# Kernel optimization log

Measured on AMD Instinct MI355X. Metric: run time of the kernel, lower is better.

Reference implementation:

```python
import jax, jax.numpy as jnp
import numpy as np

T = 4096      # total tokens (flattened batch)
H = 4096      # input_size / hidden dim
O = 4096      # output_size_per_partition
R = 16        # max_lora_rank
L = 8         # max_loras
S = 8         # num_lora_seqs


def setup_inputs() -> dict:
    key = jax.random.key(0)
    k_x, k_w, k_b, k_a, k_bb, k_idx = jax.random.split(key, 6)
    x = jax.random.normal(k_x, (T, H), dtype=jnp.float32)
    weight = jax.random.normal(k_w, (O, H), dtype=jnp.float32) * 0.02
    bias = jax.random.normal(k_b, (O,), dtype=jnp.float32)
    lora_a = jax.random.normal(k_a, (L, H, R), dtype=jnp.float32) * 0.02
    lora_b = jax.random.normal(k_bb, (L, R, O), dtype=jnp.float32) * 0.02
    # indices[i] = (start_idx[i], lora_idx[i]); indices[-1,0] = T (end sentinel).
    # Segment i covers tokens [start[i], start[i+1]) and uses adapter lora_idx[i].
    starts = jnp.arange(S + 1, dtype=jnp.int64) * (T // S)  # monotonically increasing, covers [0, T]
    lora_ids = jax.random.randint(k_idx, (S + 1,), 0, L).astype(jnp.int64)
    indices = jnp.stack([starts, lora_ids], axis=1)  # [S+1, 2]
    return {"x": x, "weight": weight, "bias": bias,
            "lora_a": lora_a, "lora_b": lora_b, "indices": indices}


def reference(x, weight, bias, lora_a, lora_b, indices):
    # Base ColumnParallelLinear: y = x @ W^T + b
    out = jnp.dot(x, weight.T) + bias  # [T, O]

    # Map each token to the LoRA adapter of its segment (SGMV semantics).
    starts = indices[:-1, 0]      # [S]
    seg_lora = indices[:-1, 1]    # [S]
    tok = jnp.arange(x.shape[0])
    seg_of_tok = jnp.searchsorted(starts, tok, side="right") - 1  # [T]
    tok_lora = seg_lora[seg_of_tok]                               # [T]

    # Grouped low-rank GEMM: out[t] += x[t] @ A[lora(t)] @ B[lora(t)].
    # Loop over the small fixed adapter set; mask selects each adapter's tokens.
    n_loras = lora_a.shape[0]
    for l in range(n_loras):
        mask = (tok_lora == l).astype(x.dtype)[:, None]  # [T, 1]
        u = jnp.dot(x * mask, lora_a[l])                 # [T, R] (zero rows off-adapter)
        out = out + jnp.dot(u, lora_b[l])                # [T, O]
    return out
```

## Files before the change

kernel.cpp:

```cpp
#include <hip/hip_runtime.h>
#include <hip/hip_bf16.h>
#include <stdint.h>

#define T_DIM 4096
#define H_DIM 4096
#define O_DIM 4096
#define R_DIM 16
#define S_SEG 8

typedef __attribute__((ext_vector_type(8))) short bf16x8_t;
typedef __attribute__((ext_vector_type(4))) float f32x4_t;

struct ushort4_t { unsigned short x, y, z, w; };

__device__ __forceinline__ unsigned short f2bf(float f) {
  union { float f; unsigned int u; } v; v.f = f;
  unsigned int u = v.u;
  unsigned int r = (u + 0x7fffu + ((u >> 16) & 1u)) >> 16;
  return (unsigned short)r;
}

__device__ __forceinline__ void gload16(const void* g, void* l) {
  __builtin_amdgcn_global_load_lds(
      (const __attribute__((address_space(1))) unsigned int*)g,
      (__attribute__((address_space(3))) unsigned int*)l,
      16, 0, 0);
}

__device__ __forceinline__ int lora_of(const int* __restrict__ indices, int t) {
  int seg = 0;
#pragma unroll
  for (int s = 1; s < S_SEG; ++s)
    if (indices[2 * s] <= t) seg = s;
  return indices[2 * seg + 1];
}

#define SBAR() do { asm volatile("" ::: "memory"); __builtin_amdgcn_s_barrier(); asm volatile("" ::: "memory"); } while (0)
#define VMCNT8() asm volatile("s_waitcnt vmcnt(8)" ::: "memory")
#define VMCNT0() asm volatile("s_waitcnt vmcnt(0)" ::: "memory")

__global__ __launch_bounds__(256) void cvt_kernel(const float* __restrict__ in,
                                                  unsigned short* __restrict__ out,
                                                  int n) {
  int i = (blockIdx.x * 256 + threadIdx.x) * 8;
  if (i >= n) return;
  float4 a = *(const float4*)(in + i);
  float4 b = *(const float4*)(in + i + 4);
  union { unsigned short s[8]; bf16x8_t v; } r;
  r.s[0] = f2bf(a.x); r.s[1] = f2bf(a.y); r.s[2] = f2bf(a.z); r.s[3] = f2bf(a.w);
  r.s[4] = f2bf(b.x); r.s[5] = f2bf(b.y); r.s[6] = f2bf(b.z); r.s[7] = f2bf(b.w);
  *(bf16x8_t*)(out + i) = r.v;
}

__global__ __launch_bounds__(256) void transpose_a(const float* __restrict__ a,
                                                   float* __restrict__ aT) {
  int l = blockIdx.y;
  const float* al = a + (size_t)l * H_DIM * R_DIM;
  float* aTl = aT + (size_t)l * H_DIM * R_DIM;
  int base = blockIdx.x * 4096;
  for (int idx = base + threadIdx.x; idx < base + 4096; idx += 256) {
    int h = idx >> 4, r = idx & 15;
    aTl[r * H_DIM + h] = al[idx];
  }
}

__global__ __launch_bounds__(256) void fused_x_kernel(const float* __restrict__ x,
                                                      const float* __restrict__ aT,
                                                      const int* __restrict__ indices,
                                                      unsigned short* __restrict__ Xb,
                                                      float* __restrict__ u) {
  const int t0 = blockIdx.x * 4;
  const int tid = threadIdx.x;
  const int l = lora_of(indices, t0);
  const float* __restrict__ aTl = aT + (size_t)l * H_DIM * R_DIM;

  float acc[4][16];
#pragma unroll
  for (int t = 0; t < 4; ++t)
#pragma unroll
    for (int r = 0; r < 16; ++r) acc[t][r] = 0.f;

#pragma unroll
  for (int c = 0; c < 4; ++c) {
    const int h = c * 1024 + tid * 4;
    union { float4 v; float f[4]; } xv[4];
#pragma unroll
    for (int t = 0; t < 4; ++t)
      xv[t].v = *(const float4*)(x + (size_t)(t0 + t) * H_DIM + h);
#pragma unroll
    for (int t = 0; t < 4; ++t) {
      ushort4_t o;
      o.x = f2bf(xv[t].f[0]); o.y = f2bf(xv[t].f[1]);
      o.z = f2bf(xv[t].f[2]); o.w = f2bf(xv[t].f[3]);
      *(ushort4_t*)(Xb + (size_t)(t0 + t) * H_DIM + h) = o;
    }
#pragma unroll
    for (int r = 0; r < 16; ++r) {
      float4 av = *(const float4*)(aTl + (size_t)r * H_DIM + h);
#pragma unroll
      for (int t = 0; t < 4; ++t)
        acc[t][r] += xv[t].f[0] * av.x + xv[t].f[1] * av.y +
                     xv[t].f[2] * av.z + xv[t].f[3] * av.w;
    }
  }

#pragma unroll
  for (int t = 0; t < 4; ++t)
#pragma unroll
    for (int r = 0; r < 16; ++r)
#pragma unroll
      for (int off = 32; off > 0; off >>= 1)
        acc[t][r] += __shfl_xor(acc[t][r], off, 64);

  __shared__ float red[4][64];
  const int lane = tid & 63, wv = tid >> 6;
  if (lane == 0) {
#pragma unroll
    for (int t = 0; t < 4; ++t)
#pragma unroll
      for (int r = 0; r < 16; ++r) red[wv][t * 16 + r] = acc[t][r];
  }
  __syncthreads();
  if (tid < 64) {
    float s = red[0][tid] + red[1][tid] + red[2][tid] + red[3][tid];
    u[(size_t)t0 * 16 + tid] = s;
  }
}

__global__ __launch_bounds__(512) void gemm256(const unsigned short* __restrict__ A,
                                               const unsigned short* __restrict__ B,
                                               const float* __restrict__ bias,
                                               const float* __restrict__ lora_b,
                                               const int* __restrict__ indices,
                                               const float* __restrict__ u,
                                               float* __restrict__ out) {
  extern __shared__ unsigned short lds[];
  const int tid = threadIdx.x;
  const int lane = tid & 63;
  const int wid = tid >> 6;
  const int wr = wid >> 2;
  const int wc = wid & 3;
  const int row0 = blockIdx.y * 256;
  const int col0 = blockIdx.x * 256;

  f32x4_t acc[8][4];
#pragma unroll
  for (int m = 0; m < 8; ++m)
#pragma unroll
    for (int n = 0; n < 4; ++n) acc[m][n] = (f32x4_t){0.f, 0.f, 0.f, 0.f};

  const int srow = tid >> 3;
  const int kbyte = ((tid & 7) * 16) ^ (((tid >> 5) & 1) << 5);
  const unsigned short* aS0 = A + (size_t)(row0 + 0 * 64 + srow) * H_DIM + (kbyte >> 1);
  const unsigned short* aS1 = A + (size_t)(row0 + 1 * 64 + srow) * H_DIM + (kbyte >> 1);
  const unsigned short* aS2 = A + (size_t)(row0 + 2 * 64 + srow) * H_DIM + (kbyte >> 1);
  const unsigned short* aS3 = A + (size_t)(row0 + 3 * 64 + srow) * H_DIM + (kbyte >> 1);
  const unsigned short* bS0 = B + (size_t)(col0 + 0 * 64 + srow) * H_DIM + (kbyte >> 1);
  const unsigned short* bS1 = B + (size_t)(col0 + 1 * 64 + srow) * H_DIM + (kbyte >> 1);
  const unsigned short* bS2 = B + (size_t)(col0 + 2 * 64 + srow) * H_DIM + (kbyte >> 1);
  const unsigned short* bS3 = B + (size_t)(col0 + 3 * 64 + srow) * H_DIM + (kbyte >> 1);

#define STAGE(kt, d) do {                                                  \
    unsigned short* La_ = lds + (d) * 16384;                               \
    unsigned short* Lb_ = lds + 32768 + (d) * 16384;                       \
    gload16(aS0 + (kt), La_ + tid * 8);                                    \
    gload16(aS1 + (kt), La_ + 4096 + tid * 8);                             \
    gload16(aS2 + (kt), La_ + 8192 + tid * 8);                             \
    gload16(aS3 + (kt), La_ + 12288 + tid * 8);                            \
    gload16(bS0 + (kt), Lb_ + tid * 8);                                    \
    gload16(bS1 + (kt), Lb_ + 4096 + tid * 8);                             \
    gload16(bS2 + (kt), Lb_ + 8192 + tid * 8);                             \
    gload16(bS3 + (kt), Lb_ + 12288 + tid * 8);                            \
  } while (0)

  const int rA = wr * 128 + (lane & 15);
  const int rB = wc * 64 + (lane & 15);
  const int aBase = rA * 64;
  const int bBase = rB * 64;
  const int ks0 = ((((lane >> 4) * 16)) ^ ((lane & 4) << 3)) >> 1;
  const int ks1 = (((64 + (lane >> 4) * 16)) ^ ((lane & 4) << 3)) >> 1;

  STAGE(0, 0);
  STAGE(64, 1);
  VMCNT8();
  SBAR();

#pragma unroll 2
  for (int t = 0; t < H_DIM / 64; ++t) {
    const int cur = t & 1;
    const unsigned short* La = lds + cur * 16384;
    const unsigned short* Lb = lds + 32768 + cur * 16384;

    bf16x8_t b0, b1, b2, b3, a0, a1, a2, a3;
    b0 = *(const bf16x8_t*)(Lb + bBase + 0 * 1024 + ks0);
    b1 = *(const bf16x8_t*)(Lb + bBase + 1 * 1024 + ks0);
    b2 = *(const bf16x8_t*)(Lb + bBase + 2 * 1024 + ks0);
    b3 = *(const bf16x8_t*)(Lb + bBase + 3 * 1024 + ks0);
    a0 = *(const bf16x8_t*)(La + aBase + 0 * 1024 + ks0);
    a1 = *(const bf16x8_t*)(La + aBase + 1 * 1024 + ks0);
    a2 = *(const bf16x8_t*)(La + aBase + 2 * 1024 + ks0);
    a3 = *(const bf16x8_t*)(La + aBase + 3 * 1024 + ks0);
    __builtin_amdgcn_s_setprio(1);
    acc[0][0] = __builtin_amdgcn_mfma_f32_16x16x32_bf16(a0, b0, acc[0][0], 0, 0, 0);
    acc[0][1] = __builtin_amdgcn_mfma_f32_16x16x32_bf16(a0, b1, acc[0][1], 0, 0, 0);
    acc[0][2] = __builtin_amdgcn_mfma_f32_16x16x32_bf16(a0, b2, acc[0][2], 0, 0, 0);
    acc[0][3] = __builtin_amdgcn_mfma_f32_16x16x32_bf16(a0, b3, acc[0][3], 0, 0, 0);
    acc[1][0] = __builtin_amdgcn_mfma_f32_16x16x32_bf16(a1, b0, acc[1][0], 0, 0, 0);
    acc[1][1] = __builtin_amdgcn_mfma_f32_16x16x32_bf16(a1, b1, acc[1][1], 0, 0, 0);
    acc[1][2] = __builtin_amdgcn_mfma_f32_16x16x32_bf16(a1, b2, acc[1][2], 0, 0, 0);
    acc[1][3] = __builtin_amdgcn_mfma_f32_16x16x32_bf16(a1, b3, acc[1][3], 0, 0, 0);
    acc[2][0] = __builtin_amdgcn_mfma_f32_16x16x32_bf16(a2, b0, acc[2][0], 0, 0, 0);
    acc[2][1] = __builtin_amdgcn_mfma_f32_16x16x32_bf16(a2, b1, acc[2][1], 0, 0, 0);
    acc[2][2] = __builtin_amdgcn_mfma_f32_16x16x32_bf16(a2, b2, acc[2][2], 0, 0, 0);
    acc[2][3] = __builtin_amdgcn_mfma_f32_16x16x32_bf16(a2, b3, acc[2][3], 0, 0, 0);
    acc[3][0] = __builtin_amdgcn_mfma_f32_16x16x32_bf16(a3, b0, acc[3][0], 0, 0, 0);
    acc[3][1] = __builtin_amdgcn_mfma_f32_16x16x32_bf16(a3, b1, acc[3][1], 0, 0, 0);
    acc[3][2] = __builtin_amdgcn_mfma_f32_16x16x32_bf16(a3, b2, acc[3][2], 0, 0, 0);
    acc[3][3] = __builtin_amdgcn_mfma_f32_16x16x32_bf16(a3, b3, acc[3][3], 0, 0, 0);
    __builtin_amdgcn_s_setprio(0);

    bf16x8_t c0, c1, c2, c3;
    c0 = *(const bf16x8_t*)(Lb + bBase + 0 * 1024 + ks1);
    c1 = *(const bf16x8_t*)(Lb + bBase + 1 * 1024 + ks1);
    c2 = *(const bf16x8_t*)(Lb + bBase + 2 * 1024 + ks1);
    c3 = *(const bf16x8_t*)(Lb + bBase + 3 * 1024 + ks1);
    a0 = *(const bf16x8_t*)(La + aBase + 0 * 1024 + ks1);
    a1 = *(const bf16x8_t*)(La + aBase + 1 * 1024 + ks1);
    a2 = *(const bf16x8_t*)(La + aBase + 2 * 1024 + ks1);
    a3 = *(const bf16x8_t*)(La + aBase + 3 * 1024 + ks1);
    __builtin_amdgcn_s_setprio(1);
    acc[0][0] = __builtin_amdgcn_mfma_f32_16x16x32_bf16(a0, c0, acc[0][0], 0, 0, 0);
    acc[0][1] = __builtin_amdgcn_mfma_f32_16x16x32_bf16(a0, c1, acc[0][1], 0, 0, 0);
    acc[0][2] = __builtin_amdgcn_mfma_f32_16x16x32_bf16(a0, c2, acc[0][2], 0, 0, 0);
    acc[0][3] = __builtin_amdgcn_mfma_f32_16x16x32_bf16(a0, c3, acc[0][3], 0, 0, 0);
    acc[1][0] = __builtin_amdgcn_mfma_f32_16x16x32_bf16(a1, c0, acc[1][0], 0, 0, 0);
    acc[1][1] = __builtin_amdgcn_mfma_f32_16x16x32_bf16(a1, c1, acc[1][1], 0, 0, 0);
    acc[1][2] = __builtin_amdgcn_mfma_f32_16x16x32_bf16(a1, c2, acc[1][2], 0, 0, 0);
    acc[1][3] = __builtin_amdgcn_mfma_f32_16x16x32_bf16(a1, c3, acc[1][3], 0, 0, 0);
    acc[2][0] = __builtin_amdgcn_mfma_f32_16x16x32_bf16(a2, c0, acc[2][0], 0, 0, 0);
    acc[2][1] = __builtin_amdgcn_mfma_f32_16x16x32_bf16(a2, c1, acc[2][1], 0, 0, 0);
    acc[2][2] = __builtin_amdgcn_mfma_f32_16x16x32_bf16(a2, c2, acc[2][2], 0, 0, 0);
    acc[2][3] = __builtin_amdgcn_mfma_f32_16x16x32_bf16(a2, c3, acc[2][3], 0, 0, 0);
    acc[3][0] = __builtin_amdgcn_mfma_f32_16x16x32_bf16(a3, c0, acc[3][0], 0, 0, 0);
    acc[3][1] = __builtin_amdgcn_mfma_f32_16x16x32_bf16(a3, c1, acc[3][1], 0, 0, 0);
    acc[3][2] = __builtin_amdgcn_mfma_f32_16x16x32_bf16(a3, c2, acc[3][2], 0, 0, 0);
    acc[3][3] = __builtin_amdgcn_mfma_f32_16x16x32_bf16(a3, c3, acc[3][3], 0, 0, 0);
    __builtin_amdgcn_s_setprio(0);

    a0 = *(const bf16x8_t*)(La + aBase + 4 * 1024 + ks0);
    a1 = *(const bf16x8_t*)(La + aBase + 5 * 1024 + ks0);
    a2 = *(const bf16x8_t*)(La + aBase + 6 * 1024 + ks0);
    a3 = *(const bf16x8_t*)(La + aBase + 7 * 1024 + ks0);
    __builtin_amdgcn_s_setprio(1);
    acc[4][0] = __builtin_amdgcn_mfma_f32_16x16x32_bf16(a0, b0, acc[4][0], 0, 0, 0);
    acc[4][1] = __builtin_amdgcn_mfma_f32_16x16x32_bf16(a0, b1, acc[4][1], 0, 0, 0);
    acc[4][2] = __builtin_amdgcn_mfma_f32_16x16x32_bf16(a0, b2, acc[4][2], 0, 0, 0);
    acc[4][3] = __builtin_amdgcn_mfma_f32_16x16x32_bf16(a0, b3, acc[4][3], 0, 0, 0);
    acc[5][0] = __builtin_amdgcn_mfma_f32_16x16x32_bf16(a1, b0, acc[5][0], 0, 0, 0);
    acc[5][1] = __builtin_amdgcn_mfma_f32_16x16x32_bf16(a1, b1, acc[5][1], 0, 0, 0);
    acc[5][2] = __builtin_amdgcn_mfma_f32_16x16x32_bf16(a1, b2, acc[5][2], 0, 0, 0);
    acc[5][3] = __builtin_amdgcn_mfma_f32_16x16x32_bf16(a1, b3, acc[5][3], 0, 0, 0);
    acc[6][0] = __builtin_amdgcn_mfma_f32_16x16x32_bf16(a2, b0, acc[6][0], 0, 0, 0);
    acc[6][1] = __builtin_amdgcn_mfma_f32_16x16x32_bf16(a2, b1, acc[6][1], 0, 0, 0);
    acc[6][2] = __builtin_amdgcn_mfma_f32_16x16x32_bf16(a2, b2, acc[6][2], 0, 0, 0);
    acc[6][3] = __builtin_amdgcn_mfma_f32_16x16x32_bf16(a2, b3, acc[6][3], 0, 0, 0);
    acc[7][0] = __builtin_amdgcn_mfma_f32_16x16x32_bf16(a3, b0, acc[7][0], 0, 0, 0);
    acc[7][1] = __builtin_amdgcn_mfma_f32_16x16x32_bf16(a3, b1, acc[7][1], 0, 0, 0);
    acc[7][2] = __builtin_amdgcn_mfma_f32_16x16x32_bf16(a3, b2, acc[7][2], 0, 0, 0);
    acc[7][3] = __builtin_amdgcn_mfma_f32_16x16x32_bf16(a3, b3, acc[7][3], 0, 0, 0);
    __builtin_amdgcn_s_setprio(0);

    a0 = *(const bf16x8_t*)(La + aBase + 4 * 1024 + ks1);
    a1 = *(const bf16x8_t*)(La + aBase + 5 * 1024 + ks1);
    a2 = *(const bf16x8_t*)(La + aBase + 6 * 1024 + ks1);
    a3 = *(const bf16x8_t*)(La + aBase + 7 * 1024 + ks1);
    __builtin_amdgcn_s_setprio(1);
    acc[4][0] = __builtin_amdgcn_mfma_f32_16x16x32_bf16(a0, c0, acc[4][0], 0, 0, 0);
    acc[4][1] = __builtin_amdgcn_mfma_f32_16x16x32_bf16(a0, c1, acc[4][1], 0, 0, 0);
    acc[4][2] = __builtin_amdgcn_mfma_f32_16x16x32_bf16(a0, c2, acc[4][2], 0, 0, 0);
    acc[4][3] = __builtin_amdgcn_mfma_f32_16x16x32_bf16(a0, c3, acc[4][3], 0, 0, 0);
    acc[5][0] = __builtin_amdgcn_mfma_f32_16x16x32_bf16(a1, c0, acc[5][0], 0, 0, 0);
    acc[5][1] = __builtin_amdgcn_mfma_f32_16x16x32_bf16(a1, c1, acc[5][1], 0, 0, 0);
    acc[5][2] = __builtin_amdgcn_mfma_f32_16x16x32_bf16(a1, c2, acc[5][2], 0, 0, 0);
    acc[5][3] = __builtin_amdgcn_mfma_f32_16x16x32_bf16(a1, c3, acc[5][3], 0, 0, 0);
    acc[6][0] = __builtin_amdgcn_mfma_f32_16x16x32_bf16(a2, c0, acc[6][0], 0, 0, 0);
    acc[6][1] = __builtin_amdgcn_mfma_f32_16x16x32_bf16(a2, c1, acc[6][1], 0, 0, 0);
    acc[6][2] = __builtin_amdgcn_mfma_f32_16x16x32_bf16(a2, c2, acc[6][2], 0, 0, 0);
    acc[6][3] = __builtin_amdgcn_mfma_f32_16x16x32_bf16(a2, c3, acc[6][3], 0, 0, 0);
    acc[7][0] = __builtin_amdgcn_mfma_f32_16x16x32_bf16(a3, c0, acc[7][0], 0, 0, 0);
    acc[7][1] = __builtin_amdgcn_mfma_f32_16x16x32_bf16(a3, c1, acc[7][1], 0, 0, 0);
    acc[7][2] = __builtin_amdgcn_mfma_f32_16x16x32_bf16(a3, c2, acc[7][2], 0, 0, 0);
    acc[7][3] = __builtin_amdgcn_mfma_f32_16x16x32_bf16(a3, c3, acc[7][3], 0, 0, 0);
    __builtin_amdgcn_s_setprio(0);

    SBAR();
    if (t + 2 < H_DIM / 64) {
      STAGE((t + 2) * 64, cur);
      VMCNT8();
    } else {
      VMCNT0();
    }
    SBAR();
  }
#undef STAGE

  const int l = lora_of(indices, row0);
  float* uL = (float*)lds;
  float* bL = (float*)lds + 4096;
  {
    const float* ug = u + (size_t)row0 * 16;
    *(float4*)(uL + tid * 8) = *(const float4*)(ug + tid * 8);
    *(float4*)(uL + tid * 8 + 4) = *(const float4*)(ug + tid * 8 + 4);
    int br = tid >> 5, bc = (tid & 31) * 8;
    const float* bg = lora_b + ((size_t)l * R_DIM + br) * O_DIM + col0 + bc;
    *(float4*)(bL + br * 256 + bc) = *(const float4*)bg;
    *(float4*)(bL + br * 256 + bc + 4) = *(const float4*)(bg + 4);
  }
  SBAR();

  const int cl0 = wc * 64 + (lane & 15);
  const int rl0 = wr * 128 + (lane >> 4) * 4;
#pragma unroll
  for (int r = 0; r < 16; ++r) {
    float b0 = bL[r * 256 + cl0];
    float b1 = bL[r * 256 + cl0 + 16];
    float b2 = bL[r * 256 + cl0 + 32];
    float b3 = bL[r * 256 + cl0 + 48];
#pragma unroll
    for (int m = 0; m < 8; ++m)
#pragma unroll
      for (int q = 0; q < 4; ++q) {
        float uv = uL[(rl0 + m * 16 + q) * 16 + r];
        acc[m][0][q] += uv * b0;
        acc[m][1][q] += uv * b1;
        acc[m][2][q] += uv * b2;
        acc[m][3][q] += uv * b3;
      }
  }

  float bv[4];
#pragma unroll
  for (int n = 0; n < 4; ++n) bv[n] = bias[col0 + cl0 + n * 16];
#pragma unroll
  for (int m = 0; m < 8; ++m)
#pragma unroll
    for (int n = 0; n < 4; ++n)
#pragma unroll
      for (int q = 0; q < 4; ++q) {
        int row = row0 + rl0 + m * 16 + q;
        out[(size_t)row * O_DIM + (col0 + cl0 + n * 16)] = acc[m][n][q] + bv[n];
      }
}

extern "C" void kernel_launch(void* const* d_in, const int* in_sizes, int n_in,
                              void* d_out, int out_size, void* d_ws, size_t ws_size,
                              hipStream_t stream) {
  const float* x      = (const float*)d_in[0];
  const float* weight = (const float*)d_in[1];
  const float* bias   = (const float*)d_in[2];
  const float* lora_a = (const float*)d_in[3];
  const float* lora_b = (const float*)d_in[4];
  const int*   indices = (const int*)d_in[5];
  float* out = (float*)d_out;

  unsigned short* Xb = (unsigned short*)d_ws;
  unsigned short* Wb = Xb + (size_t)T_DIM * H_DIM;
  float* u = (float*)(Wb + (size_t)O_DIM * H_DIM);
  float* aT = (float*)Wb;

  hipFuncSetAttribute((const void*)gemm256,
                      hipFuncAttributeMaxDynamicSharedMemorySize, 131072);

  const int nX = T_DIM * H_DIM;
  transpose_a<<<dim3(16, 8), 256, 0, stream>>>(lora_a, aT);
  fused_x_kernel<<<T_DIM / 4, 256, 0, stream>>>(x, aT, indices, Xb, u);
  cvt_kernel<<<nX / 8 / 256, 256, 0, stream>>>(weight, Wb, nX);
  gemm256<<<dim3(O_DIM / 256, T_DIM / 256), 512, 131072, stream>>>(
      Xb, Wb, bias, lora_b, indices, u, out);
}
```

Before: 361.7 us.

## Compute LoRA shrink with bf16 MFMA and merge prep kernels; widen LDS swizzle

Replaces the fp32 scalar LoRA-A projection, which used shuffle reductions, with a bf16 MFMA kernel that reads the already converted X and a bf16 transposed A. The four prep launches become two, each splitting its blocks between small side work and the bulk bf16 conversion, so the shrink GEMM overlaps the weight conversion. The LDS XOR swizzle in the main GEMM is widened to 8 lanes to cut bank conflicts. The u projection now uses bf16 inputs, which lowers its precision.

```diff
diff --git a/kernel.cpp b/kernel.cpp
--- a/kernel.cpp
+++ b/kernel.cpp
@@ -11,8 +11,6 @@
 typedef __attribute__((ext_vector_type(8))) short bf16x8_t;
 typedef __attribute__((ext_vector_type(4))) float f32x4_t;
 
-struct ushort4_t { unsigned short x, y, z, w; };
-
 __device__ __forceinline__ unsigned short f2bf(float f) {
   union { float f; unsigned int u; } v; v.f = f;
   unsigned int u = v.u;
@@ -39,91 +37,73 @@
 #define VMCNT8() asm volatile("s_waitcnt vmcnt(8)" ::: "memory")
 #define VMCNT0() asm volatile("s_waitcnt vmcnt(0)" ::: "memory")
 
-__global__ __launch_bounds__(256) void cvt_kernel(const float* __restrict__ in,
-                                                  unsigned short* __restrict__ out,
-                                                  int n) {
-  int i = (blockIdx.x * 256 + threadIdx.x) * 8;
-  if (i >= n) return;
-  float4 a = *(const float4*)(in + i);
-  float4 b = *(const float4*)(in + i + 4);
-  union { unsigned short s[8]; bf16x8_t v; } r;
-  r.s[0] = f2bf(a.x); r.s[1] = f2bf(a.y); r.s[2] = f2bf(a.z); r.s[3] = f2bf(a.w);
-  r.s[4] = f2bf(b.x); r.s[5] = f2bf(b.y); r.s[6] = f2bf(b.z); r.s[7] = f2bf(b.w);
-  *(bf16x8_t*)(out + i) = r.v;
-}
-
-__global__ __launch_bounds__(256) void transpose_a(const float* __restrict__ a,
-                                                   float* __restrict__ aT) {
-  int l = blockIdx.y;
-  const float* al = a + (size_t)l * H_DIM * R_DIM;
-  float* aTl = aT + (size_t)l * H_DIM * R_DIM;
-  int base = blockIdx.x * 4096;
-  for (int idx = base + threadIdx.x; idx < base + 4096; idx += 256) {
-    int h = idx >> 4, r = idx & 15;
-    aTl[r * H_DIM + h] = al[idx];
-  }
-}
-
-__global__ __launch_bounds__(256) void fused_x_kernel(const float* __restrict__ x,
-                                                      const float* __restrict__ aT,
-                                                      const int* __restrict__ indices,
-                                                      unsigned short* __restrict__ Xb,
-                                                      float* __restrict__ u) {
-  const int t0 = blockIdx.x * 4;
+__global__ __launch_bounds__(256) void prep1_kernel(const float* __restrict__ x,
+                                                    const float* __restrict__ a,
+                                                    unsigned short* __restrict__ Xb,
+                                                    unsigned short* __restrict__ aTb) {
+  const int bid = blockIdx.x;
   const int tid = threadIdx.x;
-  const int l = lora_of(indices, t0);
-  const float* __restrict__ aTl = aT + (size_t)l * H_DIM * R_DIM;
-
-  float acc[4][16];
-#pragma unroll
-  for (int t = 0; t < 4; ++t)
-#pragma unroll
-    for (int r = 0; r < 16; ++r) acc[t][r] = 0.f;
-
-#pragma unroll
-  for (int c = 0; c < 4; ++c) {
-    const int h = c * 1024 + tid * 4;
-    union { float4 v; float f[4]; } xv[4];
-#pragma unroll
-    for (int t = 0; t < 4; ++t)
-      xv[t].v = *(const float4*)(x + (size_t)(t0 + t) * H_DIM + h);
-#pragma unroll
-    for (int t = 0; t < 4; ++t) {
-      ushort4_t o;
-      o.x = f2bf(xv[t].f[0]); o.y = f2bf(xv[t].f[1]);
-      o.z = f2bf(xv[t].f[2]); o.w = f2bf(xv[t].f[3]);
-      *(ushort4_t*)(Xb + (size_t)(t0 + t) * H_DIM + h) = o;
+  if (bid < 128) {
+    __shared__ float tile[16][257];
+    const int l = bid >> 4, h0 = (bid & 15) * 256;
+    const float* al = a + ((size_t)l * H_DIM + h0) * R_DIM;
+    for (int i = tid; i < 4096; i += 256)
+      tile[i & 15][i >> 4] = al[i];
+    __syncthreads();
+    const int r = tid >> 4, hh = (tid & 15) * 16;
+    unsigned short* o = aTb + ((size_t)l * R_DIM + r) * H_DIM + h0 + hh;
+#pragma unroll
+    for (int j = 0; j < 16; ++j) o[j] = f2bf(tile[r][hh + j]);
+  } else {
+    const int i = (bid - 128) * 2048 + tid * 8;
+    float4 p = *(const float4*)(x + i);
+    float4 q = *(const float4*)(x + i + 4);
+    union { unsigned short s[8]; bf16x8_t v; } rr;
+    rr.s[0] = f2bf(p.x); rr.s[1] = f2bf(p.y); rr.s[2] = f2bf(p.z); rr.s[3] = f2bf(p.w);
+    rr.s[4] = f2bf(q.x); rr.s[5] = f2bf(q.y); rr.s[6] = f2bf(q.z); rr.s[7] = f2bf(q.w);
+    *(bf16x8_t*)(Xb + i) = rr.v;
+  }
+}
+
+__global__ __launch_bounds__(256) void prep2_kernel(const float* __restrict__ weight,
+                                                    const unsigned short* __restrict__ Xb,
+                                                    const unsigned short* __restrict__ aTb,
+                                                    const int* __restrict__ indices,
+                                                    unsigned short* __restrict__ Wb,
+                                                    float* __restrict__ u) {
+  const int bid = blockIdx.x;
+  const int tid = threadIdx.x;
+  if (bid < 32) {
+    const int t0 = bid * 128;
+    const int l = lora_of(indices, t0);
+    const int lane = tid & 63, wv = tid >> 6;
+    const int trow = t0 + wv * 32;
+    const unsigned short* Arow = Xb + (size_t)(trow + (lane & 15)) * H_DIM + (lane >> 4) * 8;
+    const unsigned short* Brow = aTb + ((size_t)l * R_DIM + (lane & 15)) * H_DIM + (lane >> 4) * 8;
+    f32x4_t acc0 = (f32x4_t){0.f, 0.f, 0.f, 0.f};
+    f32x4_t acc1 = (f32x4_t){0.f, 0.f, 0.f, 0.f};
+#pragma unroll 4
+    for (int k = 0; k < H_DIM; k += 32) {
+      bf16x8_t af0 = *(const bf16x8_t*)(Arow + k);
+      bf16x8_t af1 = *(const bf16x8_t*)(Arow + (size_t)16 * H_DIM + k);
+      bf16x8_t bfr = *(const bf16x8_t*)(Brow + k);
+      acc0 = __builtin_amdgcn_mfma_f32_16x16x32_bf16(af0, bfr, acc0, 0, 0, 0);
+      acc1 = __builtin_amdgcn_mfma_f32_16x16x32_bf16(af1, bfr, acc1, 0, 0, 0);
     }
-#pragma unroll
-    for (int r = 0; r < 16; ++r) {
-      float4 av = *(const float4*)(aTl + (size_t)r * H_DIM + h);
-#pragma unroll
-      for (int t = 0; t < 4; ++t)
-        acc[t][r] += xv[t].f[0] * av.x + xv[t].f[1] * av.y +
-                     xv[t].f[2] * av.z + xv[t].f[3] * av.w;
+    const int c = lane & 15, g4 = (lane >> 4) * 4;
+#pragma unroll
+    for (int q = 0; q < 4; ++q) {
+      u[(size_t)(trow + g4 + q) * 16 + c] = acc0[q];
+      u[(size_t)(trow + 16 + g4 + q) * 16 + c] = acc1[q];
     }
-  }
-
-#pragma unroll
-  for (int t = 0; t < 4; ++t)
-#pragma unroll
-    for (int r = 0; r < 16; ++r)
-#pragma unroll
-      for (int off = 32; off > 0; off >>= 1)
-        acc[t][r] += __shfl_xor(acc[t][r], off, 64);
-
-  __shared__ float red[4][64];
-  const int lane = tid & 63, wv = tid >> 6;
-  if (lane == 0) {
-#pragma unroll
-    for (int t = 0; t < 4; ++t)
-#pragma unroll
-      for (int r = 0; r < 16; ++r) red[wv][t * 16 + r] = acc[t][r];
-  }
-  __syncthreads();
-  if (tid < 64) {
-    float s = red[0][tid] + red[1][tid] + red[2][tid] + red[3][tid];
-    u[(size_t)t0 * 16 + tid] = s;
+  } else {
+    const int i = (bid - 32) * 2048 + tid * 8;
+    float4 p = *(const float4*)(weight + i);
+    float4 q = *(const float4*)(weight + i + 4);
+    union { unsigned short s[8]; bf16x8_t v; } rr;
+    rr.s[0] = f2bf(p.x); rr.s[1] = f2bf(p.y); rr.s[2] = f2bf(p.z); rr.s[3] = f2bf(p.w);
+    rr.s[4] = f2bf(q.x); rr.s[5] = f2bf(q.y); rr.s[6] = f2bf(q.z); rr.s[7] = f2bf(q.w);
+    *(bf16x8_t*)(Wb + i) = rr.v;
   }
 }
 
@@ -150,7 +130,7 @@
     for (int n = 0; n < 4; ++n) acc[m][n] = (f32x4_t){0.f, 0.f, 0.f, 0.f};
 
   const int srow = tid >> 3;
-  const int kbyte = ((tid & 7) * 16) ^ (((tid >> 5) & 1) << 5);
+  const int kbyte = ((tid & 7) * 16) ^ (((tid >> 3) & 7) << 4);
   const unsigned short* aS0 = A + (size_t)(row0 + 0 * 64 + srow) * H_DIM + (kbyte >> 1);
   const unsigned short* aS1 = A + (size_t)(row0 + 1 * 64 + srow) * H_DIM + (kbyte >> 1);
   const unsigned short* aS2 = A + (size_t)(row0 + 2 * 64 + srow) * H_DIM + (kbyte >> 1);
@@ -177,8 +157,9 @@
   const int rB = wc * 64 + (lane & 15);
   const int aBase = rA * 64;
   const int bBase = rB * 64;
-  const int ks0 = ((((lane >> 4) * 16)) ^ ((lane & 4) << 3)) >> 1;
-  const int ks1 = (((64 + (lane >> 4) * 16)) ^ ((lane & 4) << 3)) >> 1;
+  const int swz = (lane & 7) << 4;
+  const int ks0 = (((lane >> 4) * 16) ^ swz) >> 1;
+  const int ks1 = ((64 + (lane >> 4) * 16) ^ swz) >> 1;
 
   STAGE(0, 0);
   STAGE(64, 1);
@@ -366,15 +347,13 @@
   unsigned short* Xb = (unsigned short*)d_ws;
   unsigned short* Wb = Xb + (size_t)T_DIM * H_DIM;
   float* u = (float*)(Wb + (size_t)O_DIM * H_DIM);
-  float* aT = (float*)Wb;
+  unsigned short* aTb = (unsigned short*)(u + (size_t)T_DIM * 16);
 
   hipFuncSetAttribute((const void*)gemm256,
                       hipFuncAttributeMaxDynamicSharedMemorySize, 131072);
 
-  const int nX = T_DIM * H_DIM;
-  transpose_a<<<dim3(16, 8), 256, 0, stream>>>(lora_a, aT);
-  fused_x_kernel<<<T_DIM / 4, 256, 0, stream>>>(x, aT, indices, Xb, u);
-  cvt_kernel<<<nX / 8 / 256, 256, 0, stream>>>(weight, Wb, nX);
+  prep1_kernel<<<128 + 8192, 256, 0, stream>>>(x, lora_a, Xb, aTb);
+  prep2_kernel<<<32 + 8192, 256, 0, stream>>>(weight, Xb, aTb, indices, Wb, u);
   gemm256<<<dim3(O_DIM / 256, T_DIM / 256), 512, 131072, stream>>>(
       Xb, Wb, bias, lora_b, indices, u, out);
 }
```

Result: faster. 339.9 us (-6.0%).
